# Optimization experiments

Hardware: AMD Instinct MI355X
Metric: run time of the kernel (lower is better)

The kernel has to match this reference:

```python
import jax, jax.numpy as jnp
import numpy as np

B, S, T, D, H_HEADS = 2, 2048, 2048, 1024, 16
HD = D // H_HEADS
EPS = 1e-5


def _ln(x, g, b):
    m = jnp.mean(x, axis=-1, keepdims=True)
    v = jnp.mean(jnp.square(x - m), axis=-1, keepdims=True)
    return g * (x - m) * jax.lax.rsqrt(v + EPS) + b


def _mha(xq, xkv, Wq, bq, Wk, bk, Wv, bv, Wo, bo, causal):
    Bq, Lq, _ = xq.shape
    Lk = xkv.shape[1]
    q = (xq @ Wq + bq).reshape(Bq, Lq, H_HEADS, HD)
    k = (xkv @ Wk + bk).reshape(Bq, Lk, H_HEADS, HD)
    v = (xkv @ Wv + bv).reshape(Bq, Lk, H_HEADS, HD)
    scores = jnp.einsum('bqhd,bkhd->bhqk', q, k) / jnp.sqrt(jnp.asarray(HD, q.dtype))
    if causal:
        mask = jnp.tril(jnp.ones((Lq, Lk), dtype=bool))
        scores = jnp.where(mask, scores, jnp.asarray(-1e9, scores.dtype))
    p = jax.nn.softmax(scores, axis=-1)
    o = jnp.einsum('bhqk,bkhd->bqhd', p, v).reshape(Bq, Lq, D)
    return o @ Wo + bo


def setup_inputs() -> dict:
    key = jax.random.key(0)
    ks = jax.random.split(key, 24)
    s = 0.02
    def w(i):
        return jax.random.normal(ks[i], (D, D), jnp.float32) * s
    inp = {
        'S0': jax.random.normal(ks[20], (B, S, D), jnp.float32),
        'H': jax.random.normal(ks[21], (B, T, D), jnp.float32),
        'Wq1': w(0), 'bq1': jnp.zeros((D,)), 'Wk1': w(1), 'bk1': jnp.zeros((D,)),
        'Wv1': w(2), 'bv1': jnp.zeros((D,)), 'Wo1': w(3), 'bo1': jnp.zeros((D,)),
        'ln1_g': jnp.ones((D,)), 'ln1_b': jnp.zeros((D,)),
        'Wq2': w(4), 'bq2': jnp.zeros((D,)), 'Wk2': w(5), 'bk2': jnp.zeros((D,)),
        'Wv2': w(6), 'bv2': jnp.zeros((D,)), 'Wo2': w(7), 'bo2': jnp.zeros((D,)),
        'ln2_g': jnp.ones((D,)), 'ln2_b': jnp.zeros((D,)),
        'Wf': w(8), 'bf': jnp.zeros((D,)),
        'ln3_g': jnp.ones((D,)), 'ln3_b': jnp.zeros((D,)),
    }
    return inp


def reference(S0, H, Wq1, bq1, Wk1, bk1, Wv1, bv1, Wo1, bo1, ln1_g, ln1_b,
              Wq2, bq2, Wk2, bk2, Wv2, bv2, Wo2, bo2, ln2_g, ln2_b,
              Wf, bf, ln3_g, ln3_b):
    # masked (causal) self-attention + add&norm
    a1 = _mha(S0, S0, Wq1, bq1, Wk1, bk1, Wv1, bv1, Wo1, bo1, causal=True)
    S1 = _ln(S0 + a1, ln1_g, ln1_b)
    # cross-attention over encoder output H + add&norm
    a2 = _mha(S1, H, Wq2, bq2, Wk2, bk2, Wv2, bv2, Wo2, bo2, causal=False)
    S2 = _ln(S1 + a2, ln2_g, ln2_b)
    # FFN (single Linear) + add&norm
    S3 = _ln(S2 + (S2 @ Wf + bf), ln3_g, ln3_b)
    return S3
```

## Files before the change

kernel.cpp:

```cpp
#include <hip/hip_runtime.h>
#include <hip/hip_bf16.h>
#include <cstdint>
#include <cstddef>


#define D_DIM 1024
#define SEQ   2048
#define NHEAD 16
#define HDIM  64
#define MROWS 4096

typedef __attribute__((ext_vector_type(8)))  short bf16x8;
typedef __attribute__((ext_vector_type(4)))  float f32x4;
typedef __attribute__((ext_vector_type(16))) float f32x16;
typedef __attribute__((ext_vector_type(4)))  unsigned int u32x4;

static __device__ __forceinline__ short f2bf(float x) {
    __hip_bfloat16 h = __float2bfloat16(x);
    return *reinterpret_cast<short*>(&h);
}

static __device__ __forceinline__ unsigned int cvtpk(float lo, float hi2) {
    unsigned int r;
    asm("v_cvt_pk_bf16_f32 %0, %1, %2" : "=v"(r) : "v"(lo), "v"(hi2));
    return r;
}

#define GLOAD_LDS16(g, l)                                                     \
    __builtin_amdgcn_global_load_lds(                                         \
        (const __attribute__((address_space(1))) unsigned int*)(g),           \
        (__attribute__((address_space(3))) unsigned int*)(l), 16, 0, 0)

struct WPtrs { const float* p[9]; };

__global__ __launch_bounds__(256) void transpose_conv_kernel(
    WPtrs wp, short* __restrict__ Wt)
{
    __shared__ float tl[64][65];
    const int t = threadIdx.x;
    const float* src = wp.p[blockIdx.z];
    short* dst = Wt + (size_t)blockIdx.z * D_DIM * D_DIM;
    const int r0 = blockIdx.x * 64;
    const int c0 = blockIdx.y * 64;
    #pragma unroll
    for (int i = 0; i < 4; ++i) {
        int row = i * 16 + (t >> 4);
        int col = (t & 15) * 4;
        float4 v = *(const float4*)(src + (size_t)(r0 + row) * D_DIM + c0 + col);
        tl[row][col + 0] = v.x; tl[row][col + 1] = v.y;
        tl[row][col + 2] = v.z; tl[row][col + 3] = v.w;
    }
    __syncthreads();
    #pragma unroll
    for (int i = 0; i < 4; ++i) {
        int nrow = i * 16 + (t >> 4);
        int kcol = (t & 15) * 4;
        ushort4 o;
        o.x = (unsigned short)f2bf(tl[kcol + 0][nrow]);
        o.y = (unsigned short)f2bf(tl[kcol + 1][nrow]);
        o.z = (unsigned short)f2bf(tl[kcol + 2][nrow]);
        o.w = (unsigned short)f2bf(tl[kcol + 3][nrow]);
        *(ushort4*)(dst + (size_t)(c0 + nrow) * D_DIM + r0 + kcol) = o;
    }
}

__global__ __launch_bounds__(256) void conv_kernel(
    const float* __restrict__ src, short* __restrict__ dst)
{
    size_t i = ((size_t)blockIdx.x * 256 + threadIdx.x) * 8;
    float4 a = *(const float4*)(src + i);
    float4 b = *(const float4*)(src + i + 4);
    bf16x8 o;
    o[0] = f2bf(a.x); o[1] = f2bf(a.y); o[2] = f2bf(a.z); o[3] = f2bf(a.w);
    o[4] = f2bf(b.x); o[5] = f2bf(b.y); o[6] = f2bf(b.z); o[7] = f2bf(b.w);
    *(bf16x8*)(dst + i) = o;
}

#define GEMM_CORE(A_, Bt_)                                                    \
    __shared__ short As[128 * 32];                                            \
    __shared__ short Bs[128 * 32];                                            \
    const int t = threadIdx.x;                                                \
    const int wave = t >> 6, lane = t & 63;                                   \
    const int wm = wave >> 1, wn = wave & 1;                                  \
    const int m0 = blockIdx.x * 128, n0 = blockIdx.y * 128;                   \
    const int l15 = lane & 15, l4 = lane >> 4;                                \
    const int lrow = lane >> 2, lcol = (lane & 3) * 8;                        \
    f32x4 acc[4][4] = {};                                                     \
    for (int k0 = 0; k0 < D_DIM; k0 += 32) {                                  \
        __syncthreads();                                                      \
        _Pragma("unroll")                                                     \
        for (int c = 0; c < 2; ++c) {                                         \
            int chunk = wave + c * 4;                                         \
            int row = chunk * 16 + lrow;                                      \
            GLOAD_LDS16(A_  + (size_t)(m0 + row) * D_DIM + k0 + lcol,         \
                        As + chunk * 512 + lane * 8);                         \
            GLOAD_LDS16(Bt_ + (size_t)(n0 + row) * D_DIM + k0 + lcol,         \
                        Bs + chunk * 512 + lane * 8);                         \
        }                                                                     \
        __syncthreads();                                                      \
        bf16x8 af[4], bfr[4];                                                 \
        const int kq = l4 * 8;                                                \
        _Pragma("unroll")                                                     \
        for (int i = 0; i < 4; ++i)                                           \
            af[i] = *(const bf16x8*)&As[(wm * 64 + i * 16 + l15) * 32 + kq];  \
        _Pragma("unroll")                                                     \
        for (int j = 0; j < 4; ++j)                                           \
            bfr[j] = *(const bf16x8*)&Bs[(wn * 64 + j * 16 + l15) * 32 + kq]; \
        _Pragma("unroll")                                                     \
        for (int i = 0; i < 4; ++i)                                           \
            _Pragma("unroll")                                                 \
            for (int j = 0; j < 4; ++j)                                       \
                acc[i][j] = __builtin_amdgcn_mfma_f32_16x16x32_bf16(          \
                    af[i], bfr[j], acc[i][j], 0, 0, 0);                       \
    }                                                                         \
    const int rbase = m0 + wm * 64;                                           \
    const int cbase = n0 + wn * 64;

__global__ __launch_bounds__(256) void gemm_resid_kernel(
    const short* __restrict__ A, const short* __restrict__ Bt,
    const float* __restrict__ bias, const float* __restrict__ resid,
    float* __restrict__ Cout)
{
    __shared__ short As[128 * 32];
    __shared__ short Bs[64 * 32];
    const int t = threadIdx.x;
    const int wave = t >> 6, lane = t & 63;
    const int wm = wave >> 1, wn = wave & 1;
    const int m0 = blockIdx.x * 128, n0 = blockIdx.y * 64;
    const int l15 = lane & 15, l4 = lane >> 4;
    const int lrow = lane >> 2, lcol = (lane & 3) * 8;
    f32x4 acc[4][2] = {};
    for (int k0 = 0; k0 < D_DIM; k0 += 32) {
        __syncthreads();
        #pragma unroll
        for (int c = 0; c < 2; ++c) {
            int chunk = wave + c * 4;
            int row = chunk * 16 + lrow;
            GLOAD_LDS16(A + (size_t)(m0 + row) * D_DIM + k0 + lcol,
                        As + chunk * 512 + lane * 8);
        }
        {
            int row = wave * 16 + lrow;
            GLOAD_LDS16(Bt + (size_t)(n0 + row) * D_DIM + k0 + lcol,
                        Bs + wave * 512 + lane * 8);
        }
        __syncthreads();
        bf16x8 af[4], bfr[2];
        const int kq = l4 * 8;
        #pragma unroll
        for (int i = 0; i < 4; ++i)
            af[i] = *(const bf16x8*)&As[(wm * 64 + i * 16 + l15) * 32 + kq];
        #pragma unroll
        for (int j = 0; j < 2; ++j)
            bfr[j] = *(const bf16x8*)&Bs[(wn * 32 + j * 16 + l15) * 32 + kq];
        #pragma unroll
        for (int i = 0; i < 4; ++i)
            #pragma unroll
            for (int j = 0; j < 2; ++j)
                acc[i][j] = __builtin_amdgcn_mfma_f32_16x16x32_bf16(
                    af[i], bfr[j], acc[i][j], 0, 0, 0);
    }
    const int rbase = m0 + wm * 64;
    const int cbase = n0 + wn * 32;
    float bv[2];
    #pragma unroll
    for (int j = 0; j < 2; ++j) bv[j] = bias[cbase + j * 16 + l15];
    #pragma unroll
    for (int i = 0; i < 4; ++i) {
        #pragma unroll
        for (int r = 0; r < 4; ++r) {
            const int grow = rbase + i * 16 + l4 * 4 + r;
            #pragma unroll
            for (int j = 0; j < 2; ++j) {
                const int gcol = cbase + j * 16 + l15;
                float v = acc[i][j][r] + bv[j]
                        + resid[(size_t)grow * D_DIM + gcol];
                Cout[(size_t)grow * D_DIM + gcol] = v;
            }
        }
    }
}

__global__ __launch_bounds__(256) void gemm_qkv_kernel(
    const short* __restrict__ A, const short* __restrict__ Bt,
    const float* __restrict__ bias,
    short* __restrict__ Qh, short* __restrict__ Kh, short* __restrict__ Vh,
    int col0, float qscale)
{
    GEMM_CORE(A, Bt)
    float bv[4];
    #pragma unroll
    for (int j = 0; j < 4; ++j) bv[j] = bias[cbase + j * 16 + l15];
    #pragma unroll
    for (int i = 0; i < 4; ++i) {
        #pragma unroll
        for (int r = 0; r < 4; ++r) {
            const int grow = rbase + i * 16 + l4 * 4 + r;
            const int b = grow >> 11, s = grow & 2047;
            #pragma unroll
            for (int j = 0; j < 4; ++j) {
                const int vcol = col0 + cbase + j * 16 + l15;
                float v = acc[i][j][r] + bv[j];
                if (vcol < 1024) v *= qscale;
                short* dst = (vcol < 1024) ? Qh : ((vcol < 2048) ? Kh : Vh);
                const int h = (vcol >> 6) & 15, hd = vcol & 63;
                dst[((size_t)(b * 16 + h) * SEQ + s) * HDIM + hd] = f2bf(v);
            }
        }
    }
}

template<bool CAUSAL>
__global__ __launch_bounds__(256, 2) void attn_mfma_kernel(
    const short* __restrict__ Qh, const short* __restrict__ Kh,
    const short* __restrict__ Vh, short* __restrict__ O)
{
    __shared__ short Ks[2][128 * 64];
    __shared__ short Vt[2][64 * 128];

    const int t = threadIdx.x, wave = t >> 6, lane = t & 63;
    const int q_own = lane & 31, hi = lane >> 5;
    const int bh = blockIdx.y, b = bh >> 4, h = bh & 15;
    const short* Qp = Qh + (size_t)bh * SEQ * HDIM;
    const short* Kp = Kh + (size_t)bh * SEQ * HDIM;
    const short* Vp = Vh + (size_t)bh * SEQ * HDIM;
    short* Op = O + (size_t)b * SEQ * D_DIM + h * HDIM;

    const int ksrc = (t & 7) ^ ((t >> 3) & 7);
    const int vr2 = (t & 31) * 2, vg = (t >> 5) * 8;

    bf16x8 va0, vb0, va1, vb1;

    #define K_GLL(kb, buf)                                                    \
        do {                                                                  \
            _Pragma("unroll")                                                 \
            for (int c = 0; c < 4; ++c) {                                     \
                const int row = c * 32 + (t >> 3);                            \
                GLOAD_LDS16(Kp + (size_t)((kb) + row) * HDIM + ksrc * 8,      \
                            &Ks[buf][(c * 256 + t) * 8]);                     \
            }                                                                 \
        } while (0)

    #define V_LOAD(kb)                                                        \
        do {                                                                  \
            va0 = *(const bf16x8*)(Vp + (size_t)((kb) + vr2) * HDIM + vg);    \
            vb0 = *(const bf16x8*)(Vp + (size_t)((kb) + vr2 + 1) * HDIM + vg);\
            va1 = *(const bf16x8*)(Vp + (size_t)((kb) + 64 + vr2) * HDIM + vg);\
            vb1 = *(const bf16x8*)(Vp + (size_t)((kb) + 64 + vr2 + 1) * HDIM + vg);\
        } while (0)

    #define V_WRITE(buf)                                                      \
        do {                                                                  \
            _Pragma("unroll")                                                 \
            for (int j = 0; j < 8; ++j) {                                     \
                const int hd = vg + j;                                        \
                unsigned int p0 = ((unsigned int)(unsigned short)vb0[j] << 16)\
                                | (unsigned short)va0[j];                     \
                *(unsigned int*)&Vt[buf][(hd * 128 + vr2) ^ ((hd & 7) << 3)] = p0;\
                unsigned int p1 = ((unsigned int)(unsigned short)vb1[j] << 16)\
                                | (unsigned short)va1[j];                     \
                *(unsigned int*)&Vt[buf][(hd * 128 + 64 + vr2) ^ ((hd & 7) << 3)] = p1;\
            }                                                                 \
        } while (0)

    const int npm = CAUSAL ? 2 : 1;
    for (int pm = 0; pm < npm; ++pm) {
        const int qt = CAUSAL ? (pm == 0 ? (int)blockIdx.x : 15 - (int)blockIdx.x)
                              : (int)blockIdx.x;
        const int q0 = qt * 128;
        const int qw = q0 + wave * 32;

        bf16x8 qf[4];
        #pragma unroll
        for (int s = 0; s < 4; ++s)
            qf[s] = *(const bf16x8*)(Qp + (size_t)(qw + q_own) * HDIM
                                     + s * 16 + hi * 8);

        f32x16 oacc[2] = {};
        float m_ = -3e38f, l_ = 0.f;
        const int nkt = CAUSAL ? (qt + 1) : (SEQ / 128);

        if (pm) __syncthreads();

        K_GLL(0, 0);
        V_LOAD(0);
        V_WRITE(0);
        __syncthreads();

        for (int kt = 0; kt < nkt; ++kt) {
            const int cur = kt & 1, nxt = cur ^ 1;
            const int kbase = kt * 128;
            const bool have_next = (kt + 1 < nkt);

            if (have_next) {
                K_GLL(kbase + 128, nxt);
                V_LOAD(kbase + 128);
            }

            f32x16 sc[4] = {};
            __builtin_amdgcn_s_setprio(1);
            #pragma unroll
            for (int kt2 = 0; kt2 < 4; ++kt2) {
                const int krow = kt2 * 32 + q_own;
                #pragma unroll
                for (int s = 0; s < 4; ++s) {
                    bf16x8 kf = *(const bf16x8*)&Ks[cur]
                        [(krow * 64 + s * 16 + hi * 8) ^ ((krow & 7) << 3)];
                    sc[kt2] = __builtin_amdgcn_mfma_f32_32x32x16_bf16(
                        kf, qf[s], sc[kt2], 0, 0, 0);
                }
            }
            __builtin_amdgcn_s_setprio(0);

            if (CAUSAL && (kbase + 127 > qw)) {
                #pragma unroll
                for (int kt2 = 0; kt2 < 4; ++kt2)
                    #pragma unroll
                    for (int rr = 0; rr < 16; ++rr) {
                        const int k = kbase + kt2 * 32
                                    + (rr & 3) + 8 * (rr >> 2) + 4 * hi;
                        if (k > qw + q_own) sc[kt2][rr] = -1e30f;
                    }
            }

            float pmax = sc[0][0];
            #pragma unroll
            for (int kt2 = 0; kt2 < 4; ++kt2) {
                float p0 = fmaxf(fmaxf(sc[kt2][0], sc[kt2][1]),
                                 fmaxf(sc[kt2][2], sc[kt2][3]));
                float p1 = fmaxf(fmaxf(sc[kt2][4], sc[kt2][5]),
                                 fmaxf(sc[kt2][6], sc[kt2][7]));
                float p2 = fmaxf(fmaxf(sc[kt2][8], sc[kt2][9]),
                                 fmaxf(sc[kt2][10], sc[kt2][11]));
                float p3 = fmaxf(fmaxf(sc[kt2][12], sc[kt2][13]),
                                 fmaxf(sc[kt2][14], sc[kt2][15]));
                float q01 = fmaxf(p0, p1), q23 = fmaxf(p2, p3);
                pmax = (kt2 == 0) ? fmaxf(q01, q23)
                                  : fmaxf(pmax, fmaxf(q01, q23));
            }
            pmax = fmaxf(pmax, __shfl_xor(pmax, 32));

            if (!__all(pmax - m_ <= 8.0f)) {
                const float mnew = fmaxf(m_, pmax);
                const float corr = exp2f(m_ - mnew);
                l_ *= corr;
                #pragma unroll
                for (int ht = 0; ht < 2; ++ht)
                    #pragma unroll
                    for (int rr = 0; rr < 16; ++rr)
                        oacc[ht][rr] *= corr;
                m_ = mnew;
            }

            float s_own = 0.f;
            #pragma unroll
            for (int kt2 = 0; kt2 < 4; ++kt2) {
                float t0 = 0.f, t1 = 0.f, t2 = 0.f, t3 = 0.f;
                #pragma unroll
                for (int rr = 0; rr < 4; ++rr) {
                    float a = exp2f(sc[kt2][rr]      - m_);
                    float b2 = exp2f(sc[kt2][4 + rr]  - m_);
                    float c = exp2f(sc[kt2][8 + rr]  - m_);
                    float d = exp2f(sc[kt2][12 + rr] - m_);
                    sc[kt2][rr] = a;      t0 += a;
                    sc[kt2][4 + rr] = b2; t1 += b2;
                    sc[kt2][8 + rr] = c;  t2 += c;
                    sc[kt2][12 + rr] = d; t3 += d;
                }
                s_own += (t0 + t1) + (t2 + t3);
            }
            l_ += s_own + __shfl_xor(s_own, 32);

            u32x4 paw[8];
            #pragma unroll
            for (int kt2 = 0; kt2 < 4; ++kt2) {
                const unsigned int w0a = cvtpk(sc[kt2][0],  sc[kt2][1]);
                const unsigned int w0b = cvtpk(sc[kt2][2],  sc[kt2][3]);
                const unsigned int w1a = cvtpk(sc[kt2][4],  sc[kt2][5]);
                const unsigned int w1b = cvtpk(sc[kt2][6],  sc[kt2][7]);
                const unsigned int w2a = cvtpk(sc[kt2][8],  sc[kt2][9]);
                const unsigned int w2b = cvtpk(sc[kt2][10], sc[kt2][11]);
                const unsigned int w3a = cvtpk(sc[kt2][12], sc[kt2][13]);
                const unsigned int w3b = cvtpk(sc[kt2][14], sc[kt2][15]);
                {
                    const unsigned int sA = hi ? w0a : w1a;
                    const unsigned int sB = hi ? w0b : w1b;
                    const unsigned int rA = (unsigned)__shfl_xor((int)sA, 32);
                    const unsigned int rB = (unsigned)__shfl_xor((int)sB, 32);
                    const unsigned int kA = hi ? w1a : w0a;
                    const unsigned int kB = hi ? w1b : w0b;
                    paw[kt2 * 2 + 0][0] = hi ? rA : kA;
                    paw[kt2 * 2 + 0][1] = hi ? rB : kB;
                    paw[kt2 * 2 + 0][2] = hi ? kA : rA;
                    paw[kt2 * 2 + 0][3] = hi ? kB : rB;
                }
                {
                    const unsigned int sA = hi ? w2a : w3a;
                    const unsigned int sB = hi ? w2b : w3b;
                    const unsigned int rA = (unsigned)__shfl_xor((int)sA, 32);
                    const unsigned int rB = (unsigned)__shfl_xor((int)sB, 32);
                    const unsigned int kA = hi ? w3a : w2a;
                    const unsigned int kB = hi ? w3b : w2b;
                    paw[kt2 * 2 + 1][0] = hi ? rA : kA;
                    paw[kt2 * 2 + 1][1] = hi ? rB : kB;
                    paw[kt2 * 2 + 1][2] = hi ? kA : rA;
                    paw[kt2 * 2 + 1][3] = hi ? kB : rB;
                }
            }

            __builtin_amdgcn_s_setprio(1);
            #pragma unroll
            for (int ht = 0; ht < 2; ++ht) {
                const int vrow = ht * 32 + q_own;
                #pragma unroll
                for (int ks = 0; ks < 8; ++ks) {
                    bf16x8 vf = *(const bf16x8*)&Vt[cur]
                        [(vrow * 128 + ks * 16 + hi * 8) ^ ((vrow & 7) << 3)];
                    union { u32x4 u; bf16x8 bv8; } pc;
                    pc.u = paw[ks];
                    oacc[ht] = __builtin_amdgcn_mfma_f32_32x32x16_bf16(
                        vf, pc.bv8, oacc[ht], 0, 0, 0);
                }
            }
            __builtin_amdgcn_s_setprio(0);

            if (have_next) {
                V_WRITE(nxt);
                __syncthreads();
            }
        }

        const float inv = 1.0f / l_;
        const int grow = qw + q_own;
        #pragma unroll
        for (int ht = 0; ht < 2; ++ht)
            #pragma unroll
            for (int j = 0; j < 4; ++j) {
                ushort4 o;
                o.x = (unsigned short)f2bf(oacc[ht][4 * j + 0] * inv);
                o.y = (unsigned short)f2bf(oacc[ht][4 * j + 1] * inv);
                o.z = (unsigned short)f2bf(oacc[ht][4 * j + 2] * inv);
                o.w = (unsigned short)f2bf(oacc[ht][4 * j + 3] * inv);
                *(ushort4*)&Op[(size_t)grow * D_DIM + ht * 32 + 8 * j + 4 * hi] = o;
            }
    }
    #undef K_GLL
    #undef V_LOAD
    #undef V_WRITE
}

__global__ __launch_bounds__(256) void ln_kernel(
    const float* __restrict__ X, const float* __restrict__ g,
    const float* __restrict__ bb, float* __restrict__ outf,
    short* __restrict__ outb)
{
    const int row = blockIdx.x;
    const int t = threadIdx.x;
    const float* x = X + (size_t)row * D_DIM;
    float4 v = *(const float4*)(x + (t << 2));
    float s  = v.x + v.y + v.z + v.w;
    float sq = v.x * v.x + v.y * v.y + v.z * v.z + v.w * v.w;
    #pragma unroll
    for (int off = 1; off < 64; off <<= 1) {
        s  += __shfl_xor(s, off);
        sq += __shfl_xor(sq, off);
    }
    __shared__ float ss[4], ssq[4];
    const int wid = t >> 6, lane = t & 63;
    if (lane == 0) { ss[wid] = s; ssq[wid] = sq; }
    __syncthreads();
    s  = ss[0] + ss[1] + ss[2] + ss[3];
    sq = ssq[0] + ssq[1] + ssq[2] + ssq[3];
    const float mean = s * (1.0f / 1024.0f);
    const float var  = sq * (1.0f / 1024.0f) - mean * mean;
    const float inv  = rsqrtf(var + 1e-5f);
    float4 gv = *(const float4*)(g  + (t << 2));
    float4 bv = *(const float4*)(bb + (t << 2));
    float4 o;
    o.x = gv.x * (v.x - mean) * inv + bv.x;
    o.y = gv.y * (v.y - mean) * inv + bv.y;
    o.z = gv.z * (v.z - mean) * inv + bv.z;
    o.w = gv.w * (v.w - mean) * inv + bv.w;
    if (outf) *(float4*)(outf + (size_t)row * D_DIM + (t << 2)) = o;
    if (outb) {
        ushort4 ob;
        ob.x = (unsigned short)f2bf(o.x); ob.y = (unsigned short)f2bf(o.y);
        ob.z = (unsigned short)f2bf(o.z); ob.w = (unsigned short)f2bf(o.w);
        *(ushort4*)(outb + (size_t)row * D_DIM + (t << 2)) = ob;
    }
}

extern "C" void kernel_launch(void* const* d_in, const int* in_sizes, int n_in,
                              void* d_out, int out_size, void* d_ws, size_t ws_size,
                              hipStream_t stream)
{
    (void)in_sizes; (void)n_in; (void)out_size; (void)ws_size;
    const float* S0f = (const float*)d_in[0];
    const float* Hf  = (const float*)d_in[1];
    const float* bq1 = (const float*)d_in[3];
    const float* bk1 = (const float*)d_in[5];
    const float* bv1 = (const float*)d_in[7];
    const float* bo1 = (const float*)d_in[9];
    const float* g1  = (const float*)d_in[10]; const float* b1 = (const float*)d_in[11];
    const float* bq2 = (const float*)d_in[13];
    const float* bk2 = (const float*)d_in[15];
    const float* bv2 = (const float*)d_in[17];
    const float* bo2 = (const float*)d_in[19];
    const float* g2  = (const float*)d_in[20]; const float* b2 = (const float*)d_in[21];
    const float* bff = (const float*)d_in[23];
    const float* g3  = (const float*)d_in[24]; const float* b3 = (const float*)d_in[25];

    char* ws = (char*)d_ws;
    size_t off = 0;
    auto alloc = [&](size_t bytes) { char* p = ws + off; off += (bytes + 255) & ~(size_t)255; return p; };
    short* Wt   = (short*)alloc((size_t)9 * D_DIM * D_DIM * 2);
    short* bS0  = (short*)alloc((size_t)MROWS * D_DIM * 2);
    short* bH   = (short*)alloc((size_t)MROWS * D_DIM * 2);
    short* Qhb  = (short*)alloc((size_t)MROWS * D_DIM * 2);
    short* Khb  = (short*)alloc((size_t)MROWS * D_DIM * 2);
    short* Vhb  = (short*)alloc((size_t)MROWS * D_DIM * 2);
    short* bAO  = (short*)alloc((size_t)MROWS * D_DIM * 2);
    float* X    = (float*)alloc((size_t)MROWS * D_DIM * 4);
    short* bSx  = (short*)alloc((size_t)MROWS * D_DIM * 2);
    float* cb1  = (float*)alloc(3072 * 4);
    float* cb2  = (float*)alloc(2048 * 4);

    const size_t WSTRIDE = (size_t)D_DIM * D_DIM;
    const float QSCALE = 0.125f * 1.44269504088896f;

    WPtrs wp;
    wp.p[0] = (const float*)d_in[2];
    wp.p[1] = (const float*)d_in[4];
    wp.p[2] = (const float*)d_in[6];
    wp.p[3] = (const float*)d_in[8];
    wp.p[4] = (const float*)d_in[12];
    wp.p[5] = (const float*)d_in[14];
    wp.p[6] = (const float*)d_in[16];
    wp.p[7] = (const float*)d_in[18];
    wp.p[8] = (const float*)d_in[22];
    transpose_conv_kernel<<<dim3(16, 16, 9), 256, 0, stream>>>(wp, Wt);

    conv_kernel<<<2048, 256, 0, stream>>>(S0f, bS0);
    conv_kernel<<<2048, 256, 0, stream>>>(Hf, bH);

    hipMemcpyAsync(cb1,        bq1, 4096, hipMemcpyDeviceToDevice, stream);
    hipMemcpyAsync(cb1 + 1024, bk1, 4096, hipMemcpyDeviceToDevice, stream);
    hipMemcpyAsync(cb1 + 2048, bv1, 4096, hipMemcpyDeviceToDevice, stream);
    hipMemcpyAsync(cb2,        bk2, 4096, hipMemcpyDeviceToDevice, stream);
    hipMemcpyAsync(cb2 + 1024, bv2, 4096, hipMemcpyDeviceToDevice, stream);

    const dim3 blk(256);
    const dim3 attn_grid_c(8, 2 * NHEAD);
    const dim3 attn_grid_f(16, 2 * NHEAD);
    const dim3 resid_grid(32, 16);

    gemm_qkv_kernel<<<dim3(32, 24), blk, 0, stream>>>(
        bS0, Wt, cb1, Qhb, Khb, Vhb, 0, QSCALE);
    attn_mfma_kernel<true><<<attn_grid_c, blk, 0, stream>>>(Qhb, Khb, Vhb, bAO);
    gemm_resid_kernel<<<resid_grid, blk, 0, stream>>>(
        bAO, Wt + 3 * WSTRIDE, bo1, S0f, X);
    ln_kernel<<<MROWS, blk, 0, stream>>>(X, g1, b1, X, bSx);

    gemm_qkv_kernel<<<dim3(32, 8), blk, 0, stream>>>(
        bSx, Wt + 4 * WSTRIDE, bq2, Qhb, Khb, Vhb, 0, QSCALE);
    gemm_qkv_kernel<<<dim3(32, 16), blk, 0, stream>>>(
        bH, Wt + 5 * WSTRIDE, cb2, Qhb, Khb, Vhb, 1024, QSCALE);
    attn_mfma_kernel<false><<<attn_grid_f, blk, 0, stream>>>(Qhb, Khb, Vhb, bAO);
    gemm_resid_kernel<<<resid_grid, blk, 0, stream>>>(
        bAO, Wt + 7 * WSTRIDE, bo2, X, X);
    ln_kernel<<<MROWS, blk, 0, stream>>>(X, g2, b2, X, bSx);

    gemm_resid_kernel<<<resid_grid, blk, 0, stream>>>(
        bSx, Wt + 8 * WSTRIDE, bff, X, X);
    ln_kernel<<<MROWS, blk, 0, stream>>>(X, g3, b3, (float*)d_out, nullptr);
}
```

Before: 325.5 us.

## Merge conversion launches, replace bias memcpys, remap attention grid, use permlane32 swap

Folds the two fp32-to-bf16 conversion launches into one kernel and replaces five device-to-device memcpys with a single bias-concatenation kernel, reducing launch overhead. The attention grid is flattened to 1D with a block-id remap so that consecutive blocks span different heads and batches, which changes how work is spread across XCDs and cache. In the P-to-bf16 repacking, the shfl_xor plus select sequences are replaced by v_permlane32_swap_b32, cutting cross-lane instructions in the attention inner loop. These are several independent small changes bundled together.

```diff
diff --git a/kernel.cpp b/kernel.cpp
--- a/kernel.cpp
+++ b/kernel.cpp
@@ -64,16 +64,34 @@
     }
 }
 
-__global__ __launch_bounds__(256) void conv_kernel(
-    const float* __restrict__ src, short* __restrict__ dst)
-{
-    size_t i = ((size_t)blockIdx.x * 256 + threadIdx.x) * 8;
+__global__ __launch_bounds__(256) void conv2_kernel(
+    const float* __restrict__ s0, const float* __restrict__ hx,
+    short* __restrict__ d0, short* __restrict__ d1)
+{
+    const bool second = blockIdx.x >= 2048;
+    const float* src = second ? hx : s0;
+    short* dst = second ? d1 : d0;
+    size_t i = ((size_t)(blockIdx.x - (second ? 2048 : 0)) * 256 + threadIdx.x) * 8;
     float4 a = *(const float4*)(src + i);
     float4 b = *(const float4*)(src + i + 4);
     bf16x8 o;
     o[0] = f2bf(a.x); o[1] = f2bf(a.y); o[2] = f2bf(a.z); o[3] = f2bf(a.w);
     o[4] = f2bf(b.x); o[5] = f2bf(b.y); o[6] = f2bf(b.z); o[7] = f2bf(b.w);
     *(bf16x8*)(dst + i) = o;
+}
+
+__global__ __launch_bounds__(256) void bias_concat_kernel(
+    const float* __restrict__ bq1, const float* __restrict__ bk1,
+    const float* __restrict__ bv1, const float* __restrict__ bk2,
+    const float* __restrict__ bv2, float* __restrict__ cb1,
+    float* __restrict__ cb2)
+{
+    const int i = blockIdx.x * 256 + threadIdx.x;
+    if      (i < 1024) cb1[i] = bq1[i];
+    else if (i < 2048) cb1[i] = bk1[i - 1024];
+    else if (i < 3072) cb1[i] = bv1[i - 2048];
+    else if (i < 4096) cb2[i - 3072] = bk2[i - 3072];
+    else               cb2[i - 3072] = bv2[i - 4096];
 }
 
 #define GEMM_CORE(A_, Bt_)                                                    \
@@ -220,7 +238,10 @@
 
     const int t = threadIdx.x, wave = t >> 6, lane = t & 63;
     const int q_own = lane & 31, hi = lane >> 5;
-    const int bh = blockIdx.y, b = bh >> 4, h = bh & 15;
+    const int id = blockIdx.x;
+    const int bh = ((id & 7) << 2) | ((id >> 3) & 3);
+    const int qsel = id >> 5;
+    const int b = bh >> 4, h = bh & 15;
     const short* Qp = Qh + (size_t)bh * SEQ * HDIM;
     const short* Kp = Kh + (size_t)bh * SEQ * HDIM;
     const short* Vp = Vh + (size_t)bh * SEQ * HDIM;
@@ -265,8 +286,7 @@
 
     const int npm = CAUSAL ? 2 : 1;
     for (int pm = 0; pm < npm; ++pm) {
-        const int qt = CAUSAL ? (pm == 0 ? (int)blockIdx.x : 15 - (int)blockIdx.x)
-                              : (int)blockIdx.x;
+        const int qt = CAUSAL ? (pm == 0 ? qsel : 15 - qsel) : qsel;
         const int q0 = qt * 128;
         const int qw = q0 + wave * 32;
 
@@ -374,38 +394,22 @@
             u32x4 paw[8];
             #pragma unroll
             for (int kt2 = 0; kt2 < 4; ++kt2) {
-                const unsigned int w0a = cvtpk(sc[kt2][0],  sc[kt2][1]);
-                const unsigned int w0b = cvtpk(sc[kt2][2],  sc[kt2][3]);
-                const unsigned int w1a = cvtpk(sc[kt2][4],  sc[kt2][5]);
-                const unsigned int w1b = cvtpk(sc[kt2][6],  sc[kt2][7]);
-                const unsigned int w2a = cvtpk(sc[kt2][8],  sc[kt2][9]);
-                const unsigned int w2b = cvtpk(sc[kt2][10], sc[kt2][11]);
-                const unsigned int w3a = cvtpk(sc[kt2][12], sc[kt2][13]);
-                const unsigned int w3b = cvtpk(sc[kt2][14], sc[kt2][15]);
-                {
-                    const unsigned int sA = hi ? w0a : w1a;
-                    const unsigned int sB = hi ? w0b : w1b;
-                    const unsigned int rA = (unsigned)__shfl_xor((int)sA, 32);
-                    const unsigned int rB = (unsigned)__shfl_xor((int)sB, 32);
-                    const unsigned int kA = hi ? w1a : w0a;
-                    const unsigned int kB = hi ? w1b : w0b;
-                    paw[kt2 * 2 + 0][0] = hi ? rA : kA;
-                    paw[kt2 * 2 + 0][1] = hi ? rB : kB;
-                    paw[kt2 * 2 + 0][2] = hi ? kA : rA;
-                    paw[kt2 * 2 + 0][3] = hi ? kB : rB;
-                }
-                {
-                    const unsigned int sA = hi ? w2a : w3a;
-                    const unsigned int sB = hi ? w2b : w3b;
-                    const unsigned int rA = (unsigned)__shfl_xor((int)sA, 32);
-                    const unsigned int rB = (unsigned)__shfl_xor((int)sB, 32);
-                    const unsigned int kA = hi ? w3a : w2a;
-                    const unsigned int kB = hi ? w3b : w2b;
-                    paw[kt2 * 2 + 1][0] = hi ? rA : kA;
-                    paw[kt2 * 2 + 1][1] = hi ? rB : kB;
-                    paw[kt2 * 2 + 1][2] = hi ? kA : rA;
-                    paw[kt2 * 2 + 1][3] = hi ? kB : rB;
-                }
+                unsigned int w0a = cvtpk(sc[kt2][0],  sc[kt2][1]);
+                unsigned int w0b = cvtpk(sc[kt2][2],  sc[kt2][3]);
+                unsigned int w1a = cvtpk(sc[kt2][4],  sc[kt2][5]);
+                unsigned int w1b = cvtpk(sc[kt2][6],  sc[kt2][7]);
+                unsigned int w2a = cvtpk(sc[kt2][8],  sc[kt2][9]);
+                unsigned int w2b = cvtpk(sc[kt2][10], sc[kt2][11]);
+                unsigned int w3a = cvtpk(sc[kt2][12], sc[kt2][13]);
+                unsigned int w3b = cvtpk(sc[kt2][14], sc[kt2][15]);
+                asm("v_permlane32_swap_b32 %0, %1" : "+v"(w0a), "+v"(w1a));
+                asm("v_permlane32_swap_b32 %0, %1" : "+v"(w0b), "+v"(w1b));
+                asm("v_permlane32_swap_b32 %0, %1" : "+v"(w2a), "+v"(w3a));
+                asm("v_permlane32_swap_b32 %0, %1" : "+v"(w2b), "+v"(w3b));
+                paw[kt2 * 2 + 0][0] = w0a; paw[kt2 * 2 + 0][1] = w0b;
+                paw[kt2 * 2 + 0][2] = w1a; paw[kt2 * 2 + 0][3] = w1b;
+                paw[kt2 * 2 + 1][0] = w2a; paw[kt2 * 2 + 1][1] = w2b;
+                paw[kt2 * 2 + 1][2] = w3a; paw[kt2 * 2 + 1][3] = w3b;
             }
 
             __builtin_amdgcn_s_setprio(1);
@@ -540,18 +544,12 @@
     wp.p[8] = (const float*)d_in[22];
     transpose_conv_kernel<<<dim3(16, 16, 9), 256, 0, stream>>>(wp, Wt);
 
-    conv_kernel<<<2048, 256, 0, stream>>>(S0f, bS0);
-    conv_kernel<<<2048, 256, 0, stream>>>(Hf, bH);
-
-    hipMemcpyAsync(cb1,        bq1, 4096, hipMemcpyDeviceToDevice, stream);
-    hipMemcpyAsync(cb1 + 1024, bk1, 4096, hipMemcpyDeviceToDevice, stream);
-    hipMemcpyAsync(cb1 + 2048, bv1, 4096, hipMemcpyDeviceToDevice, stream);
-    hipMemcpyAsync(cb2,        bk2, 4096, hipMemcpyDeviceToDevice, stream);
-    hipMemcpyAsync(cb2 + 1024, bv2, 4096, hipMemcpyDeviceToDevice, stream);
+    conv2_kernel<<<4096, 256, 0, stream>>>(S0f, Hf, bS0, bH);
+    bias_concat_kernel<<<20, 256, 0, stream>>>(bq1, bk1, bv1, bk2, bv2, cb1, cb2);
 
     const dim3 blk(256);
-    const dim3 attn_grid_c(8, 2 * NHEAD);
-    const dim3 attn_grid_f(16, 2 * NHEAD);
+    const dim3 attn_grid_c(256);
+    const dim3 attn_grid_f(512);
     const dim3 resid_grid(32, 16);
 
     gemm_qkv_kernel<<<dim3(32, 24), blk, 0, stream>>>(
```

Measured after the change: 302.5 us. 7.1% less time.
